# Optimization experiments

Hardware: AMD Instinct MI355X
Metric: run time of the kernel (lower is better)

## Reference

```python
import jax, jax.numpy as jnp
import numpy as np
from jax import lax

DN = ('NCHW', 'OIHW', 'NCHW')

def _dwsep(x, dw, pw_w, pw_b, stride):
    # depthwise: groups = in_channels, kernel (C,1,3,3)
    y = lax.conv_general_dilated(x, dw, (stride, stride), [(1, 1), (1, 1)],
                                 dimension_numbers=DN, feature_group_count=x.shape[1])
    # pointwise 1x1
    y = lax.conv_general_dilated(y, pw_w, (1, 1), 'VALID', dimension_numbers=DN)
    return y + pw_b[None, :, None, None]

def setup_inputs() -> dict:
    key = jax.random.key(0)
    ks = jax.random.split(key, 16)
    s = 0.1
    inp = {
        'flow_raw': jax.random.normal(ks[0], (32, 2, 480, 640), jnp.float32),
        'dw1': jax.random.normal(ks[1], (5, 1, 3, 3), jnp.float32) * s,
        'pw1_w': jax.random.normal(ks[2], (32, 5, 1, 1), jnp.float32) * s,
        'pw1_b': jnp.zeros((32,), jnp.float32),
        'dw2': jax.random.normal(ks[3], (32, 1, 3, 3), jnp.float32) * s,
        'pw2_w': jax.random.normal(ks[4], (64, 32, 1, 1), jnp.float32) * s,
        'pw2_b': jnp.zeros((64,), jnp.float32),
        'dw3': jax.random.normal(ks[5], (64, 1, 3, 3), jnp.float32) * s,
        'pw3_w': jax.random.normal(ks[6], (64, 64, 1, 1), jnp.float32) * s,
        'pw3_b': jnp.zeros((64,), jnp.float32),
        'attn_w': jax.random.normal(ks[7], (1, 64, 1, 1), jnp.float32) * s,
        'attn_b': jnp.zeros((1,), jnp.float32),
        'mlp1_w': jax.random.normal(ks[8], (32, 64), jnp.float32) * s,
        'mlp1_b': jnp.zeros((32,), jnp.float32),
        'mlp2_w': jax.random.normal(ks[9], (3, 32), jnp.float32) * s,
        'mlp2_b': jnp.zeros((3,), jnp.float32),
        'w_ih': jax.random.normal(ks[10], (96, 3), jnp.float32) * s,
        'w_hh': jax.random.normal(ks[11], (96, 32), jnp.float32) * s,
        'b_ih': jnp.zeros((96,), jnp.float32),
        'b_hh': jnp.zeros((96,), jnp.float32),
        'fc_w': jnp.zeros((3, 32), jnp.float32),  # gru_fc init to zero in torch code
        'fc_b': jnp.zeros((3,), jnp.float32),
    }
    return inp

def reference(flow_raw, dw1, pw1_w, pw1_b, dw2, pw2_w, pw2_b, dw3, pw3_w, pw3_b,
              attn_w, attn_b, mlp1_w, mlp1_b, mlp2_w, mlp2_b,
              w_ih, w_hh, b_ih, b_hh, fc_w, fc_b):
    B, _, H, W = flow_raw.shape
    # coordinate channels (x, y, r^2)
    y = jnp.linspace(-1.0, 1.0, H)
    x = jnp.linspace(-1.0, 1.0, W)
    yy, xx = jnp.meshgrid(y, x, indexing='ij')
    coords = jnp.stack([xx, yy, xx**2 + yy**2], axis=0)            # (3,H,W)
    coords_b = jnp.broadcast_to(coords[None], (B, 3, H, W))
    inp = jnp.concatenate([flow_raw, coords_b], axis=1)            # (B,5,H,W)

    f = jax.nn.elu(_dwsep(inp, dw1, pw1_w, pw1_b, 2))              # (B,32,H/2,W/2)
    f = jax.nn.elu(_dwsep(f, dw2, pw2_w, pw2_b, 2))                # (B,64,H/4,W/4)
    f = jax.nn.elu(_dwsep(f, dw3, pw3_w, pw3_b, 2))                # (B,64,H/8,W/8)

    # attention pooling
    logits = jnp.einsum('bchw,oc->bohw', f, attn_w[:, :, 0, 0]) + attn_b[None, :, None, None]
    Bs, _, Hs, Ws = logits.shape
    w = jax.nn.softmax(logits.reshape(Bs, Hs * Ws), axis=-1)       # (B, HW)
    pooled = jnp.einsum('bcn,bn->bc', f.reshape(Bs, 64, Hs * Ws), w)  # (B,64)

    # omega MLP
    h1 = jax.nn.elu(pooled @ mlp1_w.T + mlp1_b)
    omega_inst = h1 @ mlp2_w.T + mlp2_b                            # (B,3)

    # single-step GRU, h0 = 0 (PyTorch gate order: r, z, n)
    h0 = jnp.zeros((B, 32), flow_raw.dtype)
    gi = omega_inst @ w_ih.T + b_ih                                # (B,96)
    gh = h0 @ w_hh.T + b_hh
    i_r, i_z, i_n = jnp.split(gi, 3, axis=-1)
    h_r, h_z, h_n = jnp.split(gh, 3, axis=-1)
    r = jax.nn.sigmoid(i_r + h_r)
    z = jax.nn.sigmoid(i_z + h_z)
    n = jnp.tanh(i_n + r * h_n)
    h = (1.0 - z) * n + z * h0                                     # (B,32)

    delta_omega = h @ fc_w.T + fc_b
    return omega_inst + delta_omega
```

## Files before the change

### kernel.cpp

```cpp
#include <hip/hip_runtime.h>
#include <hip/hip_bf16.h>

#define H0 480
#define W0 640
#define H1 240
#define W1 320
#define H2 120
#define W2 160
#define H3 60
#define W3 80

#define W_PW1T  0
#define W_PW2T  160
#define W_PW3T  2208
#define WBUF_BYTES 65536

#define F2_PB (64 * H2 * W2)
#define F3_PB (64 * H3 * W3)
#define N3    (H3 * W3)

#define TH 8
#define TW 32
#define TILES_W 5
#define TILES_H 15
#define TILES_PB 75
#define F1COLS 65
#define NP 1105
#define LROW 66
#define LCH 1122

typedef float v2f __attribute__((ext_vector_type(2)));

__global__ __launch_bounds__(256) void k_cvt(
    const float* __restrict__ pw1, const float* __restrict__ pw2,
    const float* __restrict__ pw3, float* __restrict__ wb)
{
    int t = threadIdx.x;
    for (int i = t; i < 160;  i += 256) { int o = i / 5,  c = i % 5;  wb[W_PW1T + c*32 + o] = pw1[i]; }
    for (int i = t; i < 2048; i += 256) { int o = i >> 5, c = i & 31; wb[W_PW2T + c*64 + o] = pw2[i]; }
    for (int i = t; i < 4096; i += 256) { int o = i >> 6, c = i & 63; wb[W_PW3T + c*64 + o] = pw3[i]; }
}

__global__ __launch_bounds__(256, 3) void k_fuse12(
    const float* __restrict__ flow, const float* __restrict__ dw1,
    const float* __restrict__ b1, const float* __restrict__ dw2,
    const float* __restrict__ b2, const float* __restrict__ wb,
    float* __restrict__ out)
{
    __shared__ float f1buf[8 * LCH];

    const int t = threadIdx.x;
    const int bid = blockIdx.x;
    const int b = bid / TILES_PB;
    const int tile = bid - b * TILES_PB;
    const int oh0 = (tile / TILES_W) * TH;
    const int ow0 = (tile % TILES_W) * TW;

    const float sx = 2.f / (W0 - 1), sy = 2.f / (H0 - 1);

    float cs2[3], rs3[3], cs4[3], rs4[3];
    #pragma unroll
    for (int k = 0; k < 3; k++) {
        cs2[k] = dw1[18+k]   + dw1[21+k]   + dw1[24+k];
        rs3[k] = dw1[27+3*k] + dw1[28+3*k] + dw1[29+3*k];
        cs4[k] = dw1[36+k]   + dw1[39+k]   + dw1[42+k];
        rs4[k] = dw1[36+3*k] + dw1[37+3*k] + dw1[38+3*k];
    }
    const float ax2 = 2.f * sx, ay2 = 2.f * sy;
    float ex[3], fyc[3];
    #pragma unroll
    for (int k = 0; k < 3; k++) { ex[k] = sx*(float)(k-1) - 1.f; fyc[k] = sy*(float)(k-1) - 1.f; }
    const float AX1 = ax2*(cs2[0]+cs2[1]+cs2[2]);
    const float AX0 = cs2[0]*ex[0]+cs2[1]*ex[1]+cs2[2]*ex[2];
    const float AY1 = ay2*(rs3[0]+rs3[1]+rs3[2]);
    const float AY0 = rs3[0]*fyc[0]+rs3[1]*fyc[1]+rs3[2]*fyc[2];
    const float GX2 = ax2*ax2*(cs4[0]+cs4[1]+cs4[2]);
    const float GX1 = 2.f*ax2*(cs4[0]*ex[0]+cs4[1]*ex[1]+cs4[2]*ex[2]);
    const float GX0 = cs4[0]*ex[0]*ex[0]+cs4[1]*ex[1]*ex[1]+cs4[2]*ex[2]*ex[2];
    const float GY2 = ay2*ay2*(rs4[0]+rs4[1]+rs4[2]);
    const float GY1 = 2.f*ay2*(rs4[0]*fyc[0]+rs4[1]*fyc[1]+rs4[2]*fyc[2]);
    const float GY0 = rs4[0]*fyc[0]*fyc[0]+rs4[1]*fyc[1]*fyc[1]+rs4[2]*fyc[2]*fyc[2];

    float dd[5][5];
    float vmf[5];
    int   widx[5];
    const float* fb0 = flow + (size_t)(b*2) * (H0*W0);
    const float* fb1 = fb0 + (size_t)(H0*W0);

    #pragma unroll
    for (int i = 0; i < 5; i++) {
        int p = t + i*256; if (p > NP-1) p = NP-1;
        int tr = p / F1COLS;
        int tc = p - tr * F1COLS;
        widx[i] = tr*LROW + (tc & 1)*33 + (tc >> 1);
        int fr = 2*oh0 - 1 + tr;
        int fc = 2*ow0 - 1 + tc;
        vmf[i] = (fr >= 0 && fc >= 0) ? 1.f : 0.f;
        if (fr >= 1 && fc >= 1) {
            const float* r0 = fb0 + (size_t)(2*fr - 1) * W0 + (2*fc - 1);
            const float* r1 = fb1 + (size_t)(2*fr - 1) * W0 + (2*fc - 1);
            float a0 = 0.f, a1 = 0.f;
            #pragma unroll
            for (int ky = 0; ky < 3; ky++)
                #pragma unroll
                for (int kx = 0; kx < 3; kx++) {
                    a0 = fmaf(dw1[ky*3+kx],   r0[ky*W0+kx], a0);
                    a1 = fmaf(dw1[9+ky*3+kx], r1[ky*W0+kx], a1);
                }
            dd[i][0] = a0; dd[i][1] = a1;
            float fcf = (float)fc, frf = (float)fr;
            dd[i][2] = fmaf(AX1, fcf, AX0);
            dd[i][3] = fmaf(AY1, frf, AY0);
            dd[i][4] = fmaf(fmaf(GX2, fcf, GX1), fcf, GX0)
                     + fmaf(fmaf(GY2, frf, GY1), frf, GY0);
        } else {
            int frc = fr < 0 ? 0 : fr, fcc = fc < 0 ? 0 : fc;
            int ih0 = 2*frc - 1, iw0 = 2*fcc - 1;
            float mh[3] = { ih0 >= 0 ? 1.f : 0.f, 1.f, 1.f };
            float mw[3] = { iw0 >= 0 ? 1.f : 0.f, 1.f, 1.f };
            int ihx[3] = { ih0 < 0 ? 0 : ih0, ih0 + 1, ih0 + 2 };
            int iwx[3] = { iw0 < 0 ? 0 : iw0, iw0 + 1, iw0 + 2 };
            float a0 = 0.f, a1 = 0.f;
            #pragma unroll
            for (int ky = 0; ky < 3; ky++) {
                const float* rp0 = fb0 + (size_t)ihx[ky] * W0;
                const float* rp1 = fb1 + (size_t)ihx[ky] * W0;
                #pragma unroll
                for (int kx = 0; kx < 3; kx++) {
                    float m = mh[ky]*mw[kx];
                    a0 = fmaf(dw1[ky*3+kx],   m * rp0[iwx[kx]], a0);
                    a1 = fmaf(dw1[9+ky*3+kx], m * rp1[iwx[kx]], a1);
                }
            }
            dd[i][0] = a0; dd[i][1] = a1;
            float axv = 0.f, ayv = 0.f, arv = 0.f;
            #pragma unroll
            for (int ky = 0; ky < 3; ky++) {
                float yv = fmaf((float)(ih0 + ky), sy, -1.f);
                #pragma unroll
                for (int kx = 0; kx < 3; kx++) {
                    float xv = fmaf((float)(iw0 + kx), sx, -1.f);
                    float m = mh[ky]*mw[kx];
                    axv = fmaf(dw1[18 + ky*3 + kx], m * xv, axv);
                    ayv = fmaf(dw1[27 + ky*3 + kx], m * yv, ayv);
                    arv = fmaf(dw1[36 + ky*3 + kx], m * (xv*xv + yv*yv), arv);
                }
            }
            dd[i][2] = axv; dd[i][3] = ayv; dd[i][4] = arv;
        }
    }

    v2f acc2[32];
    #pragma unroll
    for (int o = 0; o < 32; o++) acc2[o] = *(const v2f*)(b2 + 2*o);

    const int lr = t >> 5, lc = t & 31;
    const int rbase = 2*lr*LROW + lc;

    for (int cc = 0; cc < 4; cc++) {
        #pragma unroll
        for (int j = 0; j < 8; j++) {
            int c = cc*8 + j;
            float w10 = wb[W_PW1T + c];
            float w11 = wb[W_PW1T + 32 + c];
            float w12 = wb[W_PW1T + 64 + c];
            float w13 = wb[W_PW1T + 96 + c];
            float w14 = wb[W_PW1T + 128 + c];
            float bc = b1[c];
            #pragma unroll
            for (int i = 0; i < 5; i++) {
                float v = bc;
                v = fmaf(w10, dd[i][0], v);
                v = fmaf(w11, dd[i][1], v);
                v = fmaf(w12, dd[i][2], v);
                v = fmaf(w13, dd[i][3], v);
                v = fmaf(w14, dd[i][4], v);
                float f = v > 0.f ? v : (__expf(v) - 1.f);
                f *= vmf[i];
                if (i < 4)               f1buf[j*LCH + widx[i]] = f;
                else if (t < NP - 1024)  f1buf[j*LCH + widx[4]] = f;
            }
        }
        __syncthreads();
        #pragma unroll
        for (int j = 0; j < 8; j++) {
            int c = cc*8 + j;
            const float* w9 = dw2 + c*9;
            const float* fp = f1buf + j*LCH + rbase;
            float dv = 0.f;
            #pragma unroll
            for (int r = 0; r < 3; r++) {
                dv = fmaf(w9[r*3+0], fp[r*LROW],      dv);
                dv = fmaf(w9[r*3+1], fp[r*LROW + 33], dv);
                dv = fmaf(w9[r*3+2], fp[r*LROW + 1],  dv);
            }
            const v2f* wr2 = (const v2f*)(wb + W_PW2T + c*64);
            v2f dvv = { dv, dv };
            #pragma unroll
            for (int o = 0; o < 32; o++)
                acc2[o] = __builtin_elementwise_fma(wr2[o], dvv, acc2[o]);
        }
        __syncthreads();
    }

    const int oh = oh0 + lr, ow = ow0 + lc;
    size_t obase = ((size_t)b * 64) * (H2*W2) + (size_t)oh * W2 + ow;
    #pragma unroll
    for (int o = 0; o < 32; o++) {
        float va = acc2[o].x, vb2 = acc2[o].y;
        out[obase + (size_t)(2*o)   * (H2*W2)] = va  > 0.f ? va  : (__expf(va)  - 1.f);
        out[obase + (size_t)(2*o+1) * (H2*W2)] = vb2 > 0.f ? vb2 : (__expf(vb2) - 1.f);
    }
}

__global__ __launch_bounds__(256, 4) void k_stage3(
    const float* __restrict__ in, const float* __restrict__ dw3,
    const float* __restrict__ b3, const float* __restrict__ wb,
    const float* __restrict__ attn_w, const float* __restrict__ attn_b,
    float* __restrict__ out, float* __restrict__ lg)
{
    int idx = blockIdx.x * 256 + threadIdx.x;
    int ow = idx % W3; int tmp = idx / W3; int oh = tmp % H3; int b = tmp / H3;
    int ih0 = 2*oh - 1, iw0 = 2*ow - 1;
    float mh[3] = { ih0 >= 0 ? 1.f : 0.f, 1.f, 1.f };
    float mw[3] = { iw0 >= 0 ? 1.f : 0.f, 1.f, 1.f };
    int ihx[3] = { ih0 < 0 ? 0 : ih0, ih0 + 1, ih0 + 2 };
    int iwx[3] = { iw0 < 0 ? 0 : iw0, iw0 + 1, iw0 + 2 };
    float m9[9];
    int off[9];
    #pragma unroll
    for (int ky = 0; ky < 3; ky++)
        #pragma unroll
        for (int kx = 0; kx < 3; kx++) {
            m9[ky*3 + kx] = mh[ky] * mw[kx];
            off[ky*3 + kx] = ihx[ky]*W2 + iwx[kx];
        }

    v2f acc2[32];
    #pragma unroll
    for (int o = 0; o < 32; o++) acc2[o] = *(const v2f*)(b3 + 2*o);

    const float* inb = in + (size_t)b * F2_PB;
    for (int c = 0; c < 64; c++) {
        const float* g = inb + (size_t)c * (H2*W2);
        const float* w9 = dw3 + c*9;
        float dv = 0.f;
        #pragma unroll
        for (int p = 0; p < 9; p++)
            dv = fmaf(w9[p], m9[p] * g[off[p]], dv);
        const v2f* wr2 = (const v2f*)(wb + W_PW3T + c*64);
        v2f dvv = { dv, dv };
        #pragma unroll
        for (int o = 0; o < 32; o++)
            acc2[o] = __builtin_elementwise_fma(wr2[o], dvv, acc2[o]);
    }

    size_t obase = ((size_t)b * 64) * (H3*W3) + (size_t)oh*W3 + ow;
    float logit = attn_b[0];
    #pragma unroll
    for (int o = 0; o < 32; o++) {
        float va = acc2[o].x, vb2 = acc2[o].y;
        float ea = va  > 0.f ? va  : (__expf(va)  - 1.f);
        float eb = vb2 > 0.f ? vb2 : (__expf(vb2) - 1.f);
        out[obase + (size_t)(2*o)  *(H3*W3)] = ea;
        out[obase + (size_t)(2*o+1)*(H3*W3)] = eb;
        logit = fmaf(attn_w[2*o],   ea, logit);
        logit = fmaf(attn_w[2*o+1], eb, logit);
    }
    lg[b*N3 + oh*W3 + ow] = logit;
}

__global__ __launch_bounds__(256) void k_softmax(
    float* __restrict__ lg, float* __restrict__ invs)
{
    int b = blockIdx.x, t = threadIdx.x;
    int lane = t & 63, wid = t >> 6;
    __shared__ float sm[4], ss[4];
    float* base = lg + b*N3;

    float m = -1e30f;
    for (int n = t; n < N3; n += 256) m = fmaxf(m, base[n]);
    #pragma unroll
    for (int o = 32; o; o >>= 1) m = fmaxf(m, __shfl_down(m, o, 64));
    if (lane == 0) sm[wid] = m;
    __syncthreads();
    m = fmaxf(fmaxf(sm[0], sm[1]), fmaxf(sm[2], sm[3]));

    float s = 0.f;
    for (int n = t; n < N3; n += 256) {
        float e = __expf(base[n] - m);
        base[n] = e;
        s += e;
    }
    #pragma unroll
    for (int o = 32; o; o >>= 1) s += __shfl_down(s, o, 64);
    if (lane == 0) ss[wid] = s;
    __syncthreads();
    if (t == 0) invs[b] = 1.f / (ss[0] + ss[1] + ss[2] + ss[3]);
}

__global__ __launch_bounds__(256) void k_pool(
    const float* __restrict__ f3, const float* __restrict__ lg,
    const float* __restrict__ invs, float* __restrict__ pooled)
{
    int bc = blockIdx.x;
    int b = bc >> 6, c = bc & 63;
    int t = threadIdx.x, lane = t & 63, wid = t >> 6;
    __shared__ float sr[4];

    const float4* f = (const float4*)(f3 + (size_t)b * F3_PB + (size_t)c * N3);
    const float4* w = (const float4*)(lg + b*N3);

    float s = 0.f;
    for (int i = t; i < N3/4; i += 256) {
        float4 a = f[i], e = w[i];
        s = fmaf(a.x, e.x, s); s = fmaf(a.y, e.y, s);
        s = fmaf(a.z, e.z, s); s = fmaf(a.w, e.w, s);
    }
    #pragma unroll
    for (int o = 32; o; o >>= 1) s += __shfl_down(s, o, 64);
    if (lane == 0) sr[wid] = s;
    __syncthreads();
    if (t == 0) pooled[bc] = (sr[0] + sr[1] + sr[2] + sr[3]) * invs[b];
}

__global__ __launch_bounds__(64) void k_tail(
    const float* __restrict__ pooled,
    const float* __restrict__ mlp1_w, const float* __restrict__ mlp1_b,
    const float* __restrict__ mlp2_w, const float* __restrict__ mlp2_b,
    const float* __restrict__ w_ih, const float* __restrict__ b_ih,
    const float* __restrict__ b_hh,
    const float* __restrict__ fc_w, const float* __restrict__ fc_b,
    float* __restrict__ out)
{
    __shared__ float s_pooled[64];
    __shared__ float s_h1[32];
    __shared__ float s_om[3];
    __shared__ float s_h[32];
    int t = threadIdx.x, b = blockIdx.x;

    s_pooled[t] = pooled[b*64 + t];
    __syncthreads();

    if (t < 32) {
        float a = mlp1_b[t];
        #pragma unroll 8
        for (int c = 0; c < 64; c++) a = fmaf(mlp1_w[t*64 + c], s_pooled[c], a);
        s_h1[t] = a > 0.f ? a : (__expf(a) - 1.f);
    }
    __syncthreads();
    if (t < 3) {
        float a = mlp2_b[t];
        for (int j = 0; j < 32; j++) a = fmaf(mlp2_w[t*32 + j], s_h1[j], a);
        s_om[t] = a;
    }
    __syncthreads();
    if (t < 32) {
        float gr = b_ih[t], gz = b_ih[32 + t], gn = b_ih[64 + t];
        #pragma unroll
        for (int k = 0; k < 3; k++) {
            float ok = s_om[k];
            gr = fmaf(w_ih[t*3 + k],        ok, gr);
            gz = fmaf(w_ih[(32 + t)*3 + k], ok, gz);
            gn = fmaf(w_ih[(64 + t)*3 + k], ok, gn);
        }
        float hr = b_hh[t], hz = b_hh[32 + t], hn = b_hh[64 + t];
        float r = 1.f / (1.f + __expf(-(gr + hr)));
        float z = 1.f / (1.f + __expf(-(gz + hz)));
        float nn = tanhf(gn + r * hn);
        s_h[t] = (1.f - z) * nn;
    }
    __syncthreads();
    if (t < 3) {
        float dl = fc_b[t];
        for (int j = 0; j < 32; j++) dl = fmaf(fc_w[t*32 + j], s_h[j], dl);
        out[b*3 + t] = s_om[t] + dl;
    }
}

extern "C" void kernel_launch(void* const* d_in, const int* in_sizes, int n_in,
                              void* d_out, int out_size, void* d_ws, size_t ws_size,
                              hipStream_t stream)
{
    const float* flow = (const float*)d_in[0];
    float* wb = (float*)d_ws;

    float* f2     = (float*)((char*)d_ws + WBUF_BYTES);
    float* f3     = f2 + (size_t)32 * F2_PB;
    float* lg     = f3 + (size_t)32 * F3_PB;
    float* invs   = lg + (size_t)32 * N3;
    float* pooled = invs + 32;

    k_cvt<<<1, 256, 0, stream>>>(
        (const float*)d_in[2], (const float*)d_in[5], (const float*)d_in[8], wb);

    k_fuse12<<<32 * TILES_PB, 256, 0, stream>>>(
        flow, (const float*)d_in[1], (const float*)d_in[3],
        (const float*)d_in[4], (const float*)d_in[6], wb, f2);

    k_stage3<<<(32*H3*W3)/256, 256, 0, stream>>>(
        f2, (const float*)d_in[7], (const float*)d_in[9], wb,
        (const float*)d_in[10], (const float*)d_in[11], f3, lg);

    k_softmax<<<32, 256, 0, stream>>>(lg, invs);

    k_pool<<<32*64, 256, 0, stream>>>(f3, lg, invs, pooled);

    k_tail<<<32, 64, 0, stream>>>(pooled,
        (const float*)d_in[12], (const float*)d_in[13],
        (const float*)d_in[14], (const float*)d_in[15],
        (const float*)d_in[16], (const float*)d_in[18],
        (const float*)d_in[19], (const float*)d_in[20],
        (const float*)d_in[21], (float*)d_out);
}
```

Before: 310.7 us.

## Specialize interior tiles, pack pw1 math in v2f, use linear f1 smem layout

Splits k_fuse12 into an interior fast path with no boundary masking and a masked edge path, using a templated chunk routine. The pw1 pointwise computation now processes channel pairs with packed v2f FMAs and hoists weights per chunk. The f1 shared buffer changes from an even/odd column-split layout to a linear layout so the stride-2 depthwise read can use one 8-byte load plus one scalar load per row. The linear layout risks more LDS bank conflicts on the stride-2 reads, and the two specialized paths increase code size and register pressure.

Result: slower. 349.2 us (+12.4%).

```diff
diff --git a/kernel.cpp b/kernel.cpp
--- a/kernel.cpp
+++ b/kernel.cpp
@@ -39,6 +39,72 @@
     for (int i = t; i < 160;  i += 256) { int o = i / 5,  c = i % 5;  wb[W_PW1T + c*32 + o] = pw1[i]; }
     for (int i = t; i < 2048; i += 256) { int o = i >> 5, c = i & 31; wb[W_PW2T + c*64 + o] = pw2[i]; }
     for (int i = t; i < 4096; i += 256) { int o = i >> 6, c = i & 63; wb[W_PW3T + c*64 + o] = pw3[i]; }
+}
+
+template<bool MASK>
+__device__ __forceinline__ void fuse12_chunks(
+    int t, const float (&ddv)[5][5], const float (&vmf)[5], const int (&widx)[5],
+    float* __restrict__ f1buf, const float* __restrict__ wb,
+    const float* __restrict__ b1, const float* __restrict__ dw2,
+    int rbase, v2f (&acc2)[32])
+{
+    for (int cc = 0; cc < 4; cc++) {
+        v2f W[4][5], BB[4];
+        #pragma unroll
+        for (int jp = 0; jp < 4; jp++) {
+            int c = cc*8 + 2*jp;
+            #pragma unroll
+            for (int k = 0; k < 5; k++)
+                W[jp][k] = *(const v2f*)(wb + W_PW1T + k*32 + c);
+            BB[jp] = *(const v2f*)(b1 + c);
+        }
+        #pragma unroll
+        for (int i = 0; i < 5; i++) {
+            v2f d0 = { ddv[i][0], ddv[i][0] };
+            v2f d1 = { ddv[i][1], ddv[i][1] };
+            v2f d2 = { ddv[i][2], ddv[i][2] };
+            v2f d3 = { ddv[i][3], ddv[i][3] };
+            v2f d4 = { ddv[i][4], ddv[i][4] };
+            #pragma unroll
+            for (int jp = 0; jp < 4; jp++) {
+                v2f v = BB[jp];
+                v = __builtin_elementwise_fma(W[jp][0], d0, v);
+                v = __builtin_elementwise_fma(W[jp][1], d1, v);
+                v = __builtin_elementwise_fma(W[jp][2], d2, v);
+                v = __builtin_elementwise_fma(W[jp][3], d3, v);
+                v = __builtin_elementwise_fma(W[jp][4], d4, v);
+                float f0  = v.x > 0.f ? v.x : (__expf(v.x) - 1.f);
+                float f1v = v.y > 0.f ? v.y : (__expf(v.y) - 1.f);
+                if (MASK) { f0 *= vmf[i]; f1v *= vmf[i]; }
+                if (i < 4 || t < NP - 1024) {
+                    f1buf[(2*jp)  *LCH + widx[i]] = f0;
+                    f1buf[(2*jp+1)*LCH + widx[i]] = f1v;
+                }
+            }
+        }
+        __syncthreads();
+        #pragma unroll
+        for (int j = 0; j < 8; j++) {
+            int c = cc*8 + j;
+            const float* w9 = dw2 + c*9;
+            const float* fp = f1buf + j*LCH + rbase;
+            float dv = 0.f;
+            #pragma unroll
+            for (int r = 0; r < 3; r++) {
+                v2f t01 = *(const v2f*)(fp + r*LROW);
+                float t2 = fp[r*LROW + 2];
+                dv = fmaf(w9[r*3+0], t01.x, dv);
+                dv = fmaf(w9[r*3+1], t01.y, dv);
+                dv = fmaf(w9[r*3+2], t2,    dv);
+            }
+            const v2f* wr2 = (const v2f*)(wb + W_PW2T + c*64);
+            v2f dvv = { dv, dv };
+            #pragma unroll
+            for (int o = 0; o < 32; o++)
+                acc2[o] = __builtin_elementwise_fma(wr2[o], dvv, acc2[o]);
+        }
+        __syncthreads();
+    }
 }
 
 __global__ __launch_bounds__(256, 3) void k_fuse12(
@@ -81,22 +147,24 @@
     const float GY1 = 2.f*ay2*(rs4[0]*fyc[0]+rs4[1]*fyc[1]+rs4[2]*fyc[2]);
     const float GY0 = rs4[0]*fyc[0]*fyc[0]+rs4[1]*fyc[1]*fyc[1]+rs4[2]*fyc[2]*fyc[2];
 
-    float dd[5][5];
+    float ddv[5][5];
     float vmf[5];
     int   widx[5];
     const float* fb0 = flow + (size_t)(b*2) * (H0*W0);
     const float* fb1 = fb0 + (size_t)(H0*W0);
 
-    #pragma unroll
-    for (int i = 0; i < 5; i++) {
-        int p = t + i*256; if (p > NP-1) p = NP-1;
-        int tr = p / F1COLS;
-        int tc = p - tr * F1COLS;
-        widx[i] = tr*LROW + (tc & 1)*33 + (tc >> 1);
-        int fr = 2*oh0 - 1 + tr;
-        int fc = 2*ow0 - 1 + tc;
-        vmf[i] = (fr >= 0 && fc >= 0) ? 1.f : 0.f;
-        if (fr >= 1 && fc >= 1) {
+    const bool interior = (oh0 > 0) && (ow0 > 0);
+
+    if (interior) {
+        #pragma unroll
+        for (int i = 0; i < 5; i++) {
+            int p = t + i*256; if (p > NP-1) p = NP-1;
+            int tr = p / F1COLS;
+            int tc = p - tr * F1COLS;
+            widx[i] = tr*LROW + tc;
+            vmf[i] = 1.f;
+            int fr = 2*oh0 - 1 + tr;
+            int fc = 2*ow0 - 1 + tc;
             const float* r0 = fb0 + (size_t)(2*fr - 1) * W0 + (2*fc - 1);
             const float* r1 = fb1 + (size_t)(2*fr - 1) * W0 + (2*fc - 1);
             float a0 = 0.f, a1 = 0.f;
@@ -107,46 +175,75 @@
                     a0 = fmaf(dw1[ky*3+kx],   r0[ky*W0+kx], a0);
                     a1 = fmaf(dw1[9+ky*3+kx], r1[ky*W0+kx], a1);
                 }
-            dd[i][0] = a0; dd[i][1] = a1;
+            ddv[i][0] = a0; ddv[i][1] = a1;
             float fcf = (float)fc, frf = (float)fr;
-            dd[i][2] = fmaf(AX1, fcf, AX0);
-            dd[i][3] = fmaf(AY1, frf, AY0);
-            dd[i][4] = fmaf(fmaf(GX2, fcf, GX1), fcf, GX0)
-                     + fmaf(fmaf(GY2, frf, GY1), frf, GY0);
-        } else {
-            int frc = fr < 0 ? 0 : fr, fcc = fc < 0 ? 0 : fc;
-            int ih0 = 2*frc - 1, iw0 = 2*fcc - 1;
-            float mh[3] = { ih0 >= 0 ? 1.f : 0.f, 1.f, 1.f };
-            float mw[3] = { iw0 >= 0 ? 1.f : 0.f, 1.f, 1.f };
-            int ihx[3] = { ih0 < 0 ? 0 : ih0, ih0 + 1, ih0 + 2 };
-            int iwx[3] = { iw0 < 0 ? 0 : iw0, iw0 + 1, iw0 + 2 };
-            float a0 = 0.f, a1 = 0.f;
-            #pragma unroll
-            for (int ky = 0; ky < 3; ky++) {
-                const float* rp0 = fb0 + (size_t)ihx[ky] * W0;
-                const float* rp1 = fb1 + (size_t)ihx[ky] * W0;
+            ddv[i][2] = fmaf(AX1, fcf, AX0);
+            ddv[i][3] = fmaf(AY1, frf, AY0);
+            ddv[i][4] = fmaf(fmaf(GX2, fcf, GX1), fcf, GX0)
+                      + fmaf(fmaf(GY2, frf, GY1), frf, GY0);
+        }
+    } else {
+        #pragma unroll
+        for (int i = 0; i < 5; i++) {
+            int p = t + i*256; if (p > NP-1) p = NP-1;
+            int tr = p / F1COLS;
+            int tc = p - tr * F1COLS;
+            widx[i] = tr*LROW + tc;
+            int fr = 2*oh0 - 1 + tr;
+            int fc = 2*ow0 - 1 + tc;
+            vmf[i] = (fr >= 0 && fc >= 0) ? 1.f : 0.f;
+            if (fr >= 1 && fc >= 1) {
+                const float* r0 = fb0 + (size_t)(2*fr - 1) * W0 + (2*fc - 1);
+                const float* r1 = fb1 + (size_t)(2*fr - 1) * W0 + (2*fc - 1);
+                float a0 = 0.f, a1 = 0.f;
                 #pragma unroll
-                for (int kx = 0; kx < 3; kx++) {
-                    float m = mh[ky]*mw[kx];
-                    a0 = fmaf(dw1[ky*3+kx],   m * rp0[iwx[kx]], a0);
-                    a1 = fmaf(dw1[9+ky*3+kx], m * rp1[iwx[kx]], a1);
+                for (int ky = 0; ky < 3; ky++)
+                    #pragma unroll
+                    for (int kx = 0; kx < 3; kx++) {
+                        a0 = fmaf(dw1[ky*3+kx],   r0[ky*W0+kx], a0);
+                        a1 = fmaf(dw1[9+ky*3+kx], r1[ky*W0+kx], a1);
+                    }
+                ddv[i][0] = a0; ddv[i][1] = a1;
+                float fcf = (float)fc, frf = (float)fr;
+                ddv[i][2] = fmaf(AX1, fcf, AX0);
+                ddv[i][3] = fmaf(AY1, frf, AY0);
+                ddv[i][4] = fmaf(fmaf(GX2, fcf, GX1), fcf, GX0)
+                          + fmaf(fmaf(GY2, frf, GY1), frf, GY0);
+            } else {
+                int frc = fr < 0 ? 0 : fr, fcc = fc < 0 ? 0 : fc;
+                int ih0 = 2*frc - 1, iw0 = 2*fcc - 1;
+                float mh[3] = { ih0 >= 0 ? 1.f : 0.f, 1.f, 1.f };
+                float mw[3] = { iw0 >= 0 ? 1.f : 0.f, 1.f, 1.f };
+                int ihx[3] = { ih0 < 0 ? 0 : ih0, ih0 + 1, ih0 + 2 };
+                int iwx[3] = { iw0 < 0 ? 0 : iw0, iw0 + 1, iw0 + 2 };
+                float a0 = 0.f, a1 = 0.f;
+                #pragma unroll
+                for (int ky = 0; ky < 3; ky++) {
+                    const float* rp0 = fb0 + (size_t)ihx[ky] * W0;
+                    const float* rp1 = fb1 + (size_t)ihx[ky] * W0;
+                    #pragma unroll
+                    for (int kx = 0; kx < 3; kx++) {
+                        float m = mh[ky]*mw[kx];
+                        a0 = fmaf(dw1[ky*3+kx],   m * rp0[iwx[kx]], a0);
+                        a1 = fmaf(dw1[9+ky*3+kx], m * rp1[iwx[kx]], a1);
+                    }
                 }
+                ddv[i][0] = a0; ddv[i][1] = a1;
+                float axv = 0.f, ayv = 0.f, arv = 0.f;
+                #pragma unroll
+                for (int ky = 0; ky < 3; ky++) {
+                    float yv = fmaf((float)(ih0 + ky), sy, -1.f);
+                    #pragma unroll
+                    for (int kx = 0; kx < 3; kx++) {
+                        float xv = fmaf((float)(iw0 + kx), sx, -1.f);
+                        float m = mh[ky]*mw[kx];
+                        axv = fmaf(dw1[18 + ky*3 + kx], m * xv, axv);
+                        ayv = fmaf(dw1[27 + ky*3 + kx], m * yv, ayv);
+                        arv = fmaf(dw1[36 + ky*3 + kx], m * (xv*xv + yv*yv), arv);
+                    }
+                }
+                ddv[i][2] = axv; ddv[i][3] = ayv; ddv[i][4] = arv;
             }
-            dd[i][0] = a0; dd[i][1] = a1;
-            float axv = 0.f, ayv = 0.f, arv = 0.f;
-            #pragma unroll
-            for (int ky = 0; ky < 3; ky++) {
-                float yv = fmaf((float)(ih0 + ky), sy, -1.f);
-                #pragma unroll
-                for (int kx = 0; kx < 3; kx++) {
-                    float xv = fmaf((float)(iw0 + kx), sx, -1.f);
-                    float m = mh[ky]*mw[kx];
-                    axv = fmaf(dw1[18 + ky*3 + kx], m * xv, axv);
-                    ayv = fmaf(dw1[27 + ky*3 + kx], m * yv, ayv);
-                    arv = fmaf(dw1[36 + ky*3 + kx], m * (xv*xv + yv*yv), arv);
-                }
-            }
-            dd[i][2] = axv; dd[i][3] = ayv; dd[i][4] = arv;
         }
     }
 
@@ -155,53 +252,12 @@
     for (int o = 0; o < 32; o++) acc2[o] = *(const v2f*)(b2 + 2*o);
 
     const int lr = t >> 5, lc = t & 31;
-    const int rbase = 2*lr*LROW + lc;
-
-    for (int cc = 0; cc < 4; cc++) {
-        #pragma unroll
-        for (int j = 0; j < 8; j++) {
-            int c = cc*8 + j;
-            float w10 = wb[W_PW1T + c];
-            float w11 = wb[W_PW1T + 32 + c];
-            float w12 = wb[W_PW1T + 64 + c];
-            float w13 = wb[W_PW1T + 96 + c];
-            float w14 = wb[W_PW1T + 128 + c];
-            float bc = b1[c];
-            #pragma unroll
-            for (int i = 0; i < 5; i++) {
-                float v = bc;
-                v = fmaf(w10, dd[i][0], v);
-                v = fmaf(w11, dd[i][1], v);
-                v = fmaf(w12, dd[i][2], v);
-                v = fmaf(w13, dd[i][3], v);
-                v = fmaf(w14, dd[i][4], v);
-                float f = v > 0.f ? v : (__expf(v) - 1.f);
-                f *= vmf[i];
-                if (i < 4)               f1buf[j*LCH + widx[i]] = f;
-                else if (t < NP - 1024)  f1buf[j*LCH + widx[4]] = f;
-            }
-        }
-        __syncthreads();
-        #pragma unroll
-        for (int j = 0; j < 8; j++) {
-            int c = cc*8 + j;
-            const float* w9 = dw2 + c*9;
-            const float* fp = f1buf + j*LCH + rbase;
-            float dv = 0.f;
-            #pragma unroll
-            for (int r = 0; r < 3; r++) {
-                dv = fmaf(w9[r*3+0], fp[r*LROW],      dv);
-                dv = fmaf(w9[r*3+1], fp[r*LROW + 33], dv);
-                dv = fmaf(w9[r*3+2], fp[r*LROW + 1],  dv);
-            }
-            const v2f* wr2 = (const v2f*)(wb + W_PW2T + c*64);
-            v2f dvv = { dv, dv };
-            #pragma unroll
-            for (int o = 0; o < 32; o++)
-                acc2[o] = __builtin_elementwise_fma(wr2[o], dvv, acc2[o]);
-        }
-        __syncthreads();
-    }
+    const int rbase = 2*lr*LROW + 2*lc;
+
+    if (interior)
+        fuse12_chunks<false>(t, ddv, vmf, widx, f1buf, wb, b1, dw2, rbase, acc2);
+    else
+        fuse12_chunks<true>(t, ddv, vmf, widx, f1buf, wb, b1, dw2, rbase, acc2);
 
     const int oh = oh0 + lr, ow = ow0 + lc;
     size_t obase = ((size_t)b * 64) * (H2*W2) + (size_t)oh * W2 + ow;
```
